# Performance work log

Hardware: AMD Instinct MI355X
Metric: run time of the kernel (lower is better)

Reference implementation:

```python
import jax, jax.numpy as jnp
import numpy as np
from jax import lax

S = 64        # num_sam_segments
B = 2
HIMG = 336    # full-res SAM segmap / painted map
HP = 24       # DINO patch grid (336/14)
CD = 768      # DINO feature channels
CM = 3072     # concatenated backbone channels (4 layers * 768)
RH = 48       # readout spatial size ceil(336/7)
HID = 128     # SPADE hidden_mlp_channels
EPS = 1e-12


def conv2d(x, w, b=None, pad=0):
    out = lax.conv_general_dilated(x, w, (1, 1), [(pad, pad), (pad, pad)],
                                   dimension_numbers=("NCHW", "OIHW", "NCHW"))
    if b is not None:
        out = out + b[None, :, None, None]
    return out


def paint_semantic_map(f_sem, segmap):
    # f_sem: (B, C, Hp, Wp) float; segmap: (B, H, W) int
    Bn, C, Hp, Wp = f_sem.shape
    H, W = segmap.shape[1:]
    # torch F.interpolate mode='nearest' downsample: src_idx = floor(dst_idx * in/out)
    iy = (jnp.arange(Hp) * H) // Hp
    ix = (jnp.arange(Wp) * W) // Wp
    seg_p = segmap[:, iy][:, :, ix]                      # (B, Hp, Wp)
    ids = jnp.clip(seg_p, 0, S - 1).reshape(Bn, -1)      # (B, Np)
    ids_off = (ids + jnp.arange(Bn)[:, None] * S).reshape(-1)
    flat = f_sem.transpose(0, 2, 3, 1).reshape(Bn * Hp * Wp, C)
    sums = jax.ops.segment_sum(flat, ids_off, num_segments=Bn * S)
    cnt = jax.ops.segment_sum(jnp.ones((Bn * Hp * Wp, 1), flat.dtype), ids_off,
                              num_segments=Bn * S)
    means = jnp.where(cnt > 0, sums / jnp.maximum(cnt, 1.0), 0.0).reshape(Bn, S, C)
    pix = jnp.clip(segmap, 0, S - 1)                     # (B, H, W)
    painted = means[jnp.arange(Bn)[:, None, None], pix]  # (B, H, W, C) gather
    return painted.transpose(0, 3, 1, 2)                 # (B, C, H, W)


def spade_ln(x, painted, ws, bs, wg, bg, wb, bb):
    # layer_norm over (C,H,W) per sample, no affine
    mean = jnp.mean(x, axis=(1, 2, 3), keepdims=True)
    var = jnp.mean((x - mean) ** 2, axis=(1, 2, 3), keepdims=True)
    xn = (x - mean) * lax.rsqrt(var + EPS)
    sem = jax.image.resize(painted, (x.shape[0], painted.shape[1], x.shape[2], x.shape[3]),
                           method="bilinear")
    h = jax.nn.relu(conv2d(sem, ws, bs, pad=1))
    gamma = conv2d(h, wg, bg, pad=1)
    beta = conv2d(h, wb, bb, pad=1)
    return xn * (1.0 + gamma) + beta


def setup_inputs() -> dict:
    key = jax.random.key(0)
    ks = jax.random.split(key, 16)
    n = lambda k, sh: jax.random.normal(k, sh, jnp.float32) * 0.02
    inp = {
        "x_main": jax.random.normal(ks[0], (B, CM, RH, RH), jnp.float32),
        "f_sem": jax.random.normal(ks[1], (B, CD, HP, HP), jnp.float32),
        "segmap": jax.random.randint(ks[2], (B, HIMG, HIMG), 0, S, jnp.int32),
    }
    i = 3
    for li, nf in enumerate([CM, 8, 16]):
        inp[f"ws{li}"] = n(ks[i], (HID, CD, 3, 3)); inp[f"bs{li}"] = jnp.zeros((HID,), jnp.float32)
        inp[f"wg{li}"] = n(ks[i + 1], (nf, HID, 3, 3)); inp[f"bg{li}"] = jnp.zeros((nf,), jnp.float32)
        inp[f"wb{li}"] = n(ks[i + 2], (nf, HID, 3, 3)); inp[f"bb{li}"] = jnp.zeros((nf,), jnp.float32)
        i += 3
    inp["w0"] = n(ks[12], (8, CM, 1, 1)); inp["bias0"] = jnp.zeros((8,), jnp.float32)
    inp["w1"] = n(ks[13], (16, 8, 1, 1)); inp["bias1"] = jnp.zeros((16,), jnp.float32)
    inp["w2"] = n(ks[14], (1, 16, 1, 1)); inp["bias2"] = jnp.zeros((1,), jnp.float32)
    return inp


def reference(x_main, f_sem, segmap,
              ws0, bs0, wg0, bg0, wb0, bb0,
              ws1, bs1, wg1, bg1, wb1, bb1,
              ws2, bs2, wg2, bg2, wb2, bb2,
              w0, bias0, w1, bias1, w2, bias2):
    painted = paint_semantic_map(f_sem, segmap)
    h = spade_ln(x_main, painted, ws0, bs0, wg0, bg0, wb0, bb0)
    h = jax.nn.softplus(conv2d(h, w0) + bias0[None, :, None, None])
    h = spade_ln(h, painted, ws1, bs1, wg1, bg1, wb1, bb1)
    h = jax.nn.softplus(conv2d(h, w1) + bias1[None, :, None, None])
    h = spade_ln(h, painted, ws2, bs2, wg2, bg2, wb2, bb2)
    h = jax.nn.softplus(conv2d(h, w2) + bias2[None, :, None, None])
    return h  # (B, 1, RH, RH)
```

## Files before the change

kernel.cpp:

```cpp
#include <hip/hip_runtime.h>
#include <hip/hip_bf16.h>

typedef __hip_bfloat16 bf16;
typedef __bf16 v8bf __attribute__((ext_vector_type(8)));
typedef float v4f __attribute__((ext_vector_type(4)));

#define PB 2304
#define PTOT 4608

__device__ __forceinline__ float b2f(bf16 x){ return __bfloat162float(x); }
__device__ __forceinline__ bf16 f2b(float x){ return __float2bfloat16(x); }
__device__ __forceinline__ float softplus_f(float x){
  return fmaxf(x, 0.f) + log1pf(expf(-fabsf(x)));
}
__device__ __forceinline__ float LD(const void* src, size_t i, int fl){
  return fl ? ((const float*)src)[i] : b2f(((const bf16*)src)[i]);
}

__device__ __forceinline__ void gload_lds16(const void* g, void* l){
  __builtin_amdgcn_global_load_lds(
      (const __attribute__((address_space(1))) void*)g,
      (__attribute__((address_space(3))) void*)l, 16, 0, 0);
}

__global__ __launch_bounds__(256) void k_sniff(const unsigned* __restrict__ x, int* __restrict__ flag,
                                               float* __restrict__ zp){
  int t = threadIdx.x;
  if (t < 128) zp[t] = 0.f;
  int cnt = 0;
  for (int i = t; i < 4096; i += 256){
    unsigned e = (x[i] >> 8) & 0x7F;
    if (e >= 0x38 && e <= 0x42) cnt++;
  }
  for (int off = 32; off; off >>= 1) cnt += __shfl_down(cnt, off, 64);
  __shared__ int sc[4];
  if ((t & 63) == 0) sc[t >> 6] = cnt;
  __syncthreads();
  if (t == 0) *flag = (sc[0]+sc[1]+sc[2]+sc[3] < 2048) ? 1 : 0;
}

__global__ __launch_bounds__(256) void k_cvt_small(
    const void* s4, const void* s10, const void* s16, const void* s6, const void* s8,
    const void* s12, const void* s14, const void* s18, const void* s20,
    const void* s21, const void* s22, const void* s23, const void* s24,
    const void* s25, const void* s26,
    float* __restrict__ dst, const int* __restrict__ flag, float* __restrict__ MB){
  int i = blockIdx.x*256 + threadIdx.x;
  if (i >= 40537) return;
  if (i >= 31321){ MB[i - 31321] = 0.f; return; }
  int fl = *flag;
  const void* src; size_t off;
  if      (i < 128)   { src = s4;  off = i; }
  else if (i < 256)   { src = s10; off = i - 128; }
  else if (i < 384)   { src = s16; off = i - 256; }
  else if (i < 3456)  { src = s6;  off = i - 384; }
  else if (i < 6528)  { src = s8;  off = i - 3456; }
  else if (i < 6536)  { src = s12; off = i - 6528; }
  else if (i < 6544)  { src = s14; off = i - 6536; }
  else if (i < 6560)  { src = s18; off = i - 6544; }
  else if (i < 6576)  { src = s20; off = i - 6560; }
  else if (i < 31152) { src = s21; off = i - 6576; }
  else if (i < 31160) { src = s22; off = i - 31152; }
  else if (i < 31288) { src = s23; off = i - 31160; }
  else if (i < 31304) { src = s24; off = i - 31288; }
  else if (i < 31320) { src = s25; off = i - 31304; }
  else                { src = s26; off = i - 31320; }
  dst[i] = LD(src, off, fl);
}

__global__ __launch_bounds__(256) void k_bcol(const float* __restrict__ SMALLF, float* __restrict__ BCOL){
  int t = threadIdx.x;
  const float* BG1 = SMALLF + 6528; const float* BB1 = SMALLF + 6536;
  const float* BG2 = SMALLF + 6544; const float* BB2 = SMALLF + 6560;
  const float* BB0 = SMALLF + 3456; const float* W0  = SMALLF + 6576;
  if (t < 8)       BCOL[t] = BG1[t];
  else if (t < 16) BCOL[t] = BB1[t-8];
  else if (t < 32) BCOL[t] = BG2[t-16];
  else if (t < 48) BCOL[t] = BB2[t-32];
  else if (t < 64) BCOL[t] = 0.f;
  float part[8] = {0,0,0,0,0,0,0,0};
  for (int c = t; c < 3072; c += 256){
    float bb = BB0[c];
    #pragma unroll
    for (int oc = 0; oc < 8; oc++) part[oc] += bb*W0[oc*3072 + c];
  }
  __shared__ float red[4][8];
  int wv = t >> 6, lane = t & 63;
  #pragma unroll
  for (int oc = 0; oc < 8; oc++){
    float v = part[oc];
    for (int off = 32; off; off >>= 1) v += __shfl_down(v, off, 64);
    if (lane == 0) red[wv][oc] = v;
  }
  __syncthreads();
  if (t < 8) BCOL[48 + t] = red[0][t] + red[1][t] + red[2][t] + red[3][t];
}

__global__ __launch_bounds__(256) void k_mbeta(const void* __restrict__ wb0, const int* __restrict__ flag,
                                               const float* __restrict__ w0f, float* __restrict__ MB){
  int jb = blockIdx.x, nb = blockIdx.y, t = threadIdx.x;
  int fl = *flag;
  int jl = t & 127, nh = t >> 7;
  int j = jb*128 + jl;
  int src = jl*9 + jb;
  float acc[8] = {0,0,0,0,0,0,0,0};
  int n0 = nb*128 + nh*64;
  for (int i = 0; i < 64; i++){
    int n = n0 + i;
    float wv = LD(wb0, (size_t)n*1152 + src, fl);
    #pragma unroll
    for (int oc = 0; oc < 8; oc++) acc[oc] += wv*w0f[oc*3072 + n];
  }
  #pragma unroll
  for (int oc = 0; oc < 8; oc++) atomicAdd(&MB[oc*1152 + j], acc[oc]);
}

__global__ __launch_bounds__(256) void k_wsm(const float* __restrict__ MB, bf16* __restrict__ WSMALL){
  int i = blockIdx.x*256 + threadIdx.x;
  if (i >= 9216) return;
  float v = MB[i];
  bf16 hi = f2b(v);
  WSMALL[48*1152 + i] = hi;
  WSMALL[56*1152 + i] = f2b(v - b2f(hi));
}

template<int ICW>
__global__ __launch_bounds__(256) void k_permW(const void* __restrict__ src, bf16* __restrict__ dst,
                                               int total, const int* __restrict__ flag){
  int idx = blockIdx.x*256 + threadIdx.x;
  if (idx >= total) return;
  int oc = idx / (9*ICW);
  int rr = idx % (9*ICW);
  int dyx = rr / ICW, ic = rr % ICW;
  size_t si = (size_t)(oc*ICW + ic)*9 + dyx;
  dst[idx] = f2b(LD(src, si, *flag));
}

__global__ __launch_bounds__(256) void k_permoc(const void* __restrict__ src, bf16* __restrict__ dst,
                                                const int* __restrict__ flag){
  __shared__ float lds[4608];
  int t = threadIdx.x;
  size_t base = (size_t)blockIdx.x*4608;
  int fl = *flag;
  for (int i = t; i < 4608; i += 256) lds[i] = LD(src, base + i, fl);
  __syncthreads();
  for (int i = t; i < 4608; i += 256){
    int ocl = i / 1152, r = i - ocl*1152;
    int dyx = r >> 7, ic = r & 127;
    dst[base + i] = f2b(lds[ocl*1152 + ic*9 + dyx]);
  }
}

__global__ __launch_bounds__(256) void k_permws(const void* __restrict__ ws0, const void* __restrict__ ws1,
                                                const void* __restrict__ ws2, const int* __restrict__ flag,
                                                float* __restrict__ WSP){
  __shared__ float lds[6912];
  int t = threadIdx.x;
  int oc = blockIdx.x;
  int l = oc >> 7, ocl = oc & 127;
  const void* src = l == 0 ? ws0 : (l == 1 ? ws1 : ws2);
  int fl = *flag;
  for (int i = t; i < 6912; i += 256) lds[i] = LD(src, (size_t)ocl*6912 + i, fl);
  __syncthreads();
  float* o = WSP + (size_t)oc*6912;
  for (int i = t; i < 6912; i += 256){
    int dyx = i / 768, ic = i - dyx*768;
    o[i] = lds[ic*9 + dyx];
  }
}

__global__ __launch_bounds__(256) void k_seg_means(const void* __restrict__ f_sem, const int* __restrict__ flag,
                                                   const int* __restrict__ segmap,
                                                   float* __restrict__ means){
  int s = blockIdx.x, b = blockIdx.y, t = threadIdx.x;
  int fl = *flag;
  __shared__ int sid[576];
  for (int i = t; i < 576; i += 256){
    int y = i / 24, x = i % 24;
    int v = segmap[b*336*336 + (y*14)*336 + x*14];
    sid[i] = min(max(v, 0), 63);
  }
  __syncthreads();
  float a0=0.f, a1=0.f, a2=0.f; int cnt = 0;
  for (int i = 0; i < 576; i++){
    if (sid[i] == s){
      cnt++;
      a0 += LD(f_sem, (size_t)(b*768 + t      )*576 + i, fl);
      a1 += LD(f_sem, (size_t)(b*768 + t + 256)*576 + i, fl);
      a2 += LD(f_sem, (size_t)(b*768 + t + 512)*576 + i, fl);
    }
  }
  float inv = cnt > 0 ? 1.f/(float)cnt : 0.f;
  float* o = means + (size_t)(b*64 + s)*768;
  o[t] = a0*inv; o[t+256] = a1*inv; o[t+512] = a2*inv;
}

__global__ __launch_bounds__(256) void k_tt(const float* __restrict__ WSP,
    const float* __restrict__ means, bf16* __restrict__ WTT){
  int bx = blockIdx.x;
  int dyx = bx / 24, ocb = bx % 24;
  int b = blockIdx.y, t = threadIdx.x;
  int ocg0 = ocb*16;
  __shared__ float wl[16][768];
  for (int ol = 0; ol < 16; ol++)
    for (int ic = t; ic < 768; ic += 256)
      wl[ol][ic] = WSP[(size_t)(ocg0 + ol)*6912 + (size_t)dyx*768 + ic];
  __syncthreads();
  int s = t & 63, og = t >> 6;
  const float* mr = means + ((size_t)b*64 + s)*768;
  float acc[4] = {0.f, 0.f, 0.f, 0.f};
  for (int ic = 0; ic < 768; ic += 4){
    float4 m = *reinterpret_cast<const float4*>(mr + ic);
    #pragma unroll
    for (int k = 0; k < 4; k++){
      const float* w = &wl[og + k*4][ic];
      acc[k] += m.x*w[0] + m.y*w[1] + m.z*w[2] + m.w*w[3];
    }
  }
  #pragma unroll
  for (int k = 0; k < 4; k++){
    bf16 h = f2b(acc[k]);
    size_t base = ((size_t)(b*384 + ocg0 + og + k*4))*1152 + (size_t)dyx*128 + s;
    WTT[base] = h;
    WTT[base + 64] = h;
  }
}

__global__ __launch_bounds__(192) void k_A(const int* __restrict__ segmap, bf16* __restrict__ AHL){
  int blk = blockIdx.x;
  int b = blk / PB, rem = blk % PB, yo = rem / 48, xo = rem % 48;
  __shared__ float accs[64];
  int t = threadIdx.x;
  if (t < 64) accs[t] = 0.f;
  __syncthreads();
  if (t < 169){
    int ty = t / 13, tx = t % 13;
    int jy = 7*yo - 3 + ty, jx = 7*xo - 3 + tx;
    if (jy >= 0 && jy < 336 && jx >= 0 && jx < 336){
      int wy = 7 - abs(ty - 6), wx = 7 - abs(tx - 6);
      int sv = segmap[b*336*336 + jy*336 + jx];
      sv = min(max(sv, 0), 63);
      atomicAdd(&accs[sv], (float)(wy*wx));
    }
  }
  int sumy = 0, sumx = 0;
  for (int k = 0; k < 13; k++){
    int jy = 7*yo - 3 + k; if (jy >= 0 && jy < 336) sumy += 7 - abs(k - 6);
    int jx = 7*xo - 3 + k; if (jx >= 0 && jx < 336) sumx += 7 - abs(k - 6);
  }
  __syncthreads();
  if (t < 64){
    float v = accs[t] / (float)(sumy*sumx);
    bf16 hi = f2b(v);
    AHL[(size_t)blk*128 + t] = hi;
    AHL[(size_t)blk*128 + 64 + t] = f2b(v - b2f(hi));
  }
}

__global__ __launch_bounds__(256) void k_ln_partial(const void* __restrict__ x, const int* __restrict__ flag,
                                                    float2* __restrict__ part){
  int b = blockIdx.y, blk = blockIdx.x, t = threadIdx.x;
  int fl = *flag;
  size_t base = (size_t)b*7077888 + (size_t)blk*55296;
  float s = 0.f, sq = 0.f;
  for (int i = 0; i < 216; i++){
    float v = LD(x, base + t + i*256, fl);
    s += v; sq += v*v;
  }
  for (int off = 32; off; off >>= 1){ s += __shfl_down(s, off, 64); sq += __shfl_down(sq, off, 64); }
  __shared__ float ls[4], lq[4];
  int w = t >> 6, lane = t & 63;
  if (lane == 0){ ls[w] = s; lq[w] = sq; }
  __syncthreads();
  if (t == 0) part[b*128 + blk] = make_float2(ls[0]+ls[1]+ls[2]+ls[3], lq[0]+lq[1]+lq[2]+lq[3]);
}

__global__ void k_ln_final(const float2* __restrict__ part, float* __restrict__ stats){
  int b = blockIdx.x, t = threadIdx.x;
  float2 v = part[b*128 + t];
  float s = v.x, sq = v.y;
  for (int off = 32; off; off >>= 1){ s += __shfl_down(s, off, 64); sq += __shfl_down(sq, off, 64); }
  __shared__ float ls[2], lq[2];
  if ((t & 63) == 0){ ls[t>>6] = s; lq[t>>6] = sq; }
  __syncthreads();
  if (t == 0){
    s = ls[0]+ls[1]; sq = lq[0]+lq[1];
    const float N = 7077888.f;
    float mean = s/N; float var = sq/N - mean*mean; var = fmaxf(var, 0.f);
    stats[b*2] = mean; stats[b*2+1] = rsqrtf(var + 1e-12f);
  }
}

__global__ __launch_bounds__(256) void k_spln(float* __restrict__ z, int cnt, float* __restrict__ stats){
  int b = blockIdx.x, t = threadIdx.x;
  float* p = z + (size_t)b*cnt;
  float s = 0.f, sq = 0.f;
  for (int i = t; i < cnt; i += 256){
    float v = softplus_f(p[i]);
    p[i] = v;
    s += v; sq += v*v;
  }
  for (int off = 32; off; off >>= 1){ s += __shfl_down(s, off, 64); sq += __shfl_down(sq, off, 64); }
  __shared__ float ls[4], lq[4];
  int w = t >> 6, lane = t & 63;
  if (lane == 0){ ls[w] = s; lq[w] = sq; }
  __syncthreads();
  if (t == 0){
    s = ls[0]+ls[1]+ls[2]+ls[3]; sq = lq[0]+lq[1]+lq[2]+lq[3];
    float mean = s/(float)cnt; float var = sq/(float)cnt - mean*mean; var = fmaxf(var, 0.f);
    stats[b*2] = mean; stats[b*2+1] = rsqrtf(var + 1e-12f);
  }
}

__global__ __launch_bounds__(256) void k_ln_small(const float* __restrict__ z, int cnt, float* __restrict__ stats){
  int b = blockIdx.x, t = threadIdx.x;
  const float* p = z + (size_t)b*cnt;
  float s = 0.f, sq = 0.f;
  for (int i = t; i < cnt; i += 256){ float v = p[i]; s += v; sq += v*v; }
  for (int off = 32; off; off >>= 1){ s += __shfl_down(s, off, 64); sq += __shfl_down(sq, off, 64); }
  __shared__ float ls[4], lq[4];
  int w = t >> 6, lane = t & 63;
  if (lane == 0){ ls[w] = s; lq[w] = sq; }
  __syncthreads();
  if (t == 0){
    s = ls[0]+ls[1]+ls[2]+ls[3]; sq = lq[0]+lq[1]+lq[2]+lq[3];
    float mean = s/(float)cnt; float var = sq/(float)cnt - mean*mean; var = fmaxf(var, 0.f);
    stats[b*2] = mean; stats[b*2+1] = rsqrtf(var + 1e-12f);
  }
}

template<bool RELU, typename OT>
__device__ __forceinline__ void gemm_body(
    const bf16* __restrict__ Asrc, int AS, int acol, int ICW,
    const bf16* __restrict__ W, int K, size_t wbstride,
    const float* __restrict__ bp0, const float* __restrict__ bp1, const float* __restrict__ bp2, int seg,
    OT* __restrict__ out, int N, int ncb, int ldo, const bf16* __restrict__ zpad,
    int m0, int n0, bf16 (*Al)[64], bf16 (*Bl)[64])
{
  int t = threadIdx.x;
  int wv = t >> 6, lane = t & 63;
  int lr8 = lane >> 3, sseg = (lane & 7) ^ lr8;
  int b = m0 >= PB ? 1 : 0;

  int ya[2], xa[2]; bool bv[2]; const bf16* wb[2];
  #pragma unroll
  for (int i = 0; i < 2; i++){
    int sp = (m0 - b*PB) + wv*16 + i*8 + lr8;
    ya[i] = sp / 48; xa[i] = sp % 48;
    int nrow = ncb + n0 + wv*16 + i*8 + lr8;
    bv[i] = nrow < N;
    wb[i] = W + (size_t)b*wbstride + (size_t)nrow*K + sseg*8;
  }

  int wm = (wv >> 1)*32, wn = (wv & 1)*32;
  int lrow = lane & 15, quad = lane >> 4;
  int sx = lrow & 7;
  int o0 = ((quad    ) ^ sx)*8;
  int o1 = ((quad + 4) ^ sx)*8;

  v4f acc00 = {0,0,0,0}, acc01 = {0,0,0,0}, acc10 = {0,0,0,0}, acc11 = {0,0,0,0};

  int dyx = 0, ic0 = 0;
  int ktn = K / 64;
  for (int kt = 0; kt < ktn; kt++){
    int dy = dyx/3 - 1, dx = dyx%3 - 1;
    #pragma unroll
    for (int i = 0; i < 2; i++){
      int ys = ya[i] + dy, xs = xa[i] + dx;
      const bf16* ga = (ys >= 0 && ys < 48 && xs >= 0 && xs < 48)
        ? Asrc + (size_t)(b*PB + ys*48 + xs)*AS + acol + ic0 + sseg*8 : zpad;
      gload_lds16(ga, &Al[wv*16 + i*8][0]);
      const bf16* gb = bv[i] ? wb[i] + kt*64 : zpad;
      gload_lds16(gb, &Bl[wv*16 + i*8][0]);
    }
    asm volatile("s_waitcnt vmcnt(0)" ::: "memory");
    __syncthreads();
    v8bf a00 = *reinterpret_cast<const v8bf*>(&Al[wm      + lrow][o0]);
    v8bf a10 = *reinterpret_cast<const v8bf*>(&Al[wm + 16 + lrow][o0]);
    v8bf a01 = *reinterpret_cast<const v8bf*>(&Al[wm      + lrow][o1]);
    v8bf a11 = *reinterpret_cast<const v8bf*>(&Al[wm + 16 + lrow][o1]);
    v8bf b00 = *reinterpret_cast<const v8bf*>(&Bl[wn      + lrow][o0]);
    v8bf b10 = *reinterpret_cast<const v8bf*>(&Bl[wn + 16 + lrow][o0]);
    v8bf b01 = *reinterpret_cast<const v8bf*>(&Bl[wn      + lrow][o1]);
    v8bf b11 = *reinterpret_cast<const v8bf*>(&Bl[wn + 16 + lrow][o1]);
    acc00 = __builtin_amdgcn_mfma_f32_16x16x32_bf16(a00, b00, acc00, 0, 0, 0);
    acc00 = __builtin_amdgcn_mfma_f32_16x16x32_bf16(a01, b01, acc00, 0, 0, 0);
    acc01 = __builtin_amdgcn_mfma_f32_16x16x32_bf16(a00, b10, acc01, 0, 0, 0);
    acc01 = __builtin_amdgcn_mfma_f32_16x16x32_bf16(a01, b11, acc01, 0, 0, 0);
    acc10 = __builtin_amdgcn_mfma_f32_16x16x32_bf16(a10, b00, acc10, 0, 0, 0);
    acc10 = __builtin_amdgcn_mfma_f32_16x16x32_bf16(a11, b01, acc10, 0, 0, 0);
    acc11 = __builtin_amdgcn_mfma_f32_16x16x32_bf16(a10, b10, acc11, 0, 0, 0);
    acc11 = __builtin_amdgcn_mfma_f32_16x16x32_bf16(a11, b11, acc11, 0, 0, 0);
    __syncthreads();
    ic0 += 64; if (ic0 == ICW){ ic0 = 0; dyx++; }
  }

  auto store_tile = [&](v4f a, int mi, int ni){
    int gcol = ncb + n0 + wn + ni*16 + lrow;
    if (gcol >= N) return;
    int sel = gcol / seg; sel = sel > 2 ? 2 : sel;
    const float* bp = sel == 0 ? bp0 : (sel == 1 ? bp1 : bp2);
    float bias = bp[gcol - sel*seg];
    int rowb = m0 + wm + mi*16 + quad*4;
    #pragma unroll
    for (int rg = 0; rg < 4; rg++){
      float v = a[rg] + bias;
      if (RELU) v = fmaxf(v, 0.f);
      if constexpr (sizeof(OT) == 2) out[(size_t)(rowb+rg)*ldo + (gcol - ncb)] = f2b(v);
      else                           out[(size_t)(rowb+rg)*ldo + (gcol - ncb)] = (OT)v;
    }
  };
  store_tile(acc00, 0, 0); store_tile(acc01, 0, 1);
  store_tile(acc10, 1, 0); store_tile(acc11, 1, 1);
}

template<bool RELU, typename OT>
__global__ __launch_bounds__(256) void k_gemm(
    const bf16* __restrict__ Asrc, int AS, int acol, int ICW,
    const bf16* __restrict__ W, int K, size_t wbstride,
    const float* __restrict__ bp0, const float* __restrict__ bp1, const float* __restrict__ bp2, int seg,
    OT* __restrict__ out, int N, int ncb, int ldo, const bf16* __restrict__ zpad)
{
  __shared__ __align__(16) bf16 Al[64][64];
  __shared__ __align__(16) bf16 Bl[64][64];
  gemm_body<RELU, OT>(Asrc, AS, acol, ICW, W, K, wbstride, bp0, bp1, bp2, seg,
                      out, N, ncb, ldo, zpad, blockIdx.x*64, blockIdx.y*64, Al, Bl);
}

__global__ __launch_bounds__(256) void k_gsmall(
    const bf16* __restrict__ HS, const bf16* __restrict__ WSMALL, const float* __restrict__ BCOL,
    float* __restrict__ GBS, const bf16* __restrict__ zpad)
{
  __shared__ __align__(16) bf16 Al[64][64];
  __shared__ __align__(16) bf16 Bl[64][64];
  int y = blockIdx.y;
  int acol = y == 0 ? 128 : (y == 1 ? 256 : 0);
  const bf16* W = WSMALL + (y == 0 ? 0 : (y == 1 ? 16*1152 : 48*1152));
  const float* bp = BCOL + (y == 0 ? 0 : (y == 1 ? 16 : 48));
  float* out = GBS + (y == 0 ? 0 : (y == 1 ? 16 : 48));
  int N = y == 1 ? 32 : 16;
  gemm_body<false, float>(HS, 384, acol, 128, W, 1152, 0, bp, bp, bp, 9999,
                          out, N, 0, 64, zpad, blockIdx.x*64, 0, Al, Bl);
}

__global__ __launch_bounds__(256, 4) void k_gg(
    const bf16* __restrict__ HS, const bf16* __restrict__ WG0, const float* __restrict__ BG0,
    bf16* __restrict__ GAMMA, const bf16* __restrict__ zpad)
{
  __shared__ __align__(16) bf16 Al[128][64];
  __shared__ __align__(16) bf16 Bl[128][64];
  int t = threadIdx.x;
  int m0 = blockIdx.x*128, n0 = blockIdx.y*128;
  int b = m0 >= PB ? 1 : 0;
  int wv = t >> 6, lane = t & 63;
  int lr8 = lane >> 3, sseg = (lane & 7) ^ lr8;
  int spbase = m0 - b*PB;

  int ya[4], xa[4];
  #pragma unroll
  for (int i = 0; i < 4; i++){
    int sp = spbase + wv*32 + i*8 + lr8;
    ya[i] = sp / 48; xa[i] = sp % 48;
  }
  const bf16* wgb = WG0 + (size_t)(n0 + wv*32 + lr8)*1152 + sseg*8;

  int wm = wv*32, lrow = lane & 15, quad = lane >> 4;
  int sx = lrow & 7;

  v4f acc[2][8];
  #pragma unroll
  for (int mi = 0; mi < 2; mi++)
    #pragma unroll
    for (int ni = 0; ni < 8; ni++) acc[mi][ni] = (v4f){0,0,0,0};

  for (int kt = 0; kt < 18; kt++){
    int dyx = kt >> 1, icr = (kt & 1) << 6;
    int dy = dyx/3 - 1, dx = dyx%3 - 1;
    #pragma unroll
    for (int i = 0; i < 4; i++){
      int ys = ya[i] + dy, xs = xa[i] + dx;
      const bf16* ga = (ys >= 0 && ys < 48 && xs >= 0 && xs < 48)
        ? HS + (size_t)(b*PB + ys*48 + xs)*384 + icr + sseg*8 : zpad;
      gload_lds16(ga, &Al[wv*32 + i*8][0]);
      gload_lds16(wgb + (size_t)(i*8)*1152 + dyx*128 + icr, &Bl[wv*32 + i*8][0]);
    }
    asm volatile("s_waitcnt vmcnt(0)" ::: "memory");
    __syncthreads();
    #pragma unroll
    for (int kh = 0; kh < 2; kh++){
      int oa = ((kh*4 + quad) ^ sx)*8;
      v8bf a0 = *reinterpret_cast<const v8bf*>(&Al[wm      + lrow][oa]);
      v8bf a1 = *reinterpret_cast<const v8bf*>(&Al[wm + 16 + lrow][oa]);
      #pragma unroll
      for (int ni = 0; ni < 8; ni++){
        v8bf bn = *reinterpret_cast<const v8bf*>(&Bl[ni*16 + lrow][oa]);
        acc[0][ni] = __builtin_amdgcn_mfma_f32_16x16x32_bf16(a0, bn, acc[0][ni], 0, 0, 0);
        acc[1][ni] = __builtin_amdgcn_mfma_f32_16x16x32_bf16(a1, bn, acc[1][ni], 0, 0, 0);
      }
    }
    __syncthreads();
  }

  #pragma unroll
  for (int mi = 0; mi < 2; mi++){
    int pr = m0 + wm + mi*16 + quad*4;
    #pragma unroll
    for (int ni = 0; ni < 8; ni++){
      int gc = n0 + ni*16 + lrow;
      float bg = BG0[gc];
      #pragma unroll
      for (int rg = 0; rg < 4; rg++)
        GAMMA[(size_t)(pr + rg)*3072 + gc] = f2b(acc[mi][ni][rg] + bg);
    }
  }
}

__global__ __launch_bounds__(256) void k_zc(
    const void* __restrict__ x, const bf16* __restrict__ GAMMA, const int* __restrict__ flag,
    const float* __restrict__ stats, const float* __restrict__ w0f, float* __restrict__ z0)
{
  __shared__ bf16 gmT[64][66];
  __shared__ float w0l[8][64];
  __shared__ float red[4][64][8];
  int t = threadIdx.x;
  int p0 = blockIdx.x*64, cb = blockIdx.y;
  int b = p0 / PB;
  int spbase = p0 - b*PB;
  int fl = *flag;
  float mean = stats[b*2], rstd = stats[b*2+1];
  int px = t & 63, cg = t >> 6;
  int pxs = t >> 6, cl = t & 63;

  float acc[8] = {0,0,0,0,0,0,0,0};
  for (int ct = 0; ct < 6; ct++){
    int c0 = cb*384 + ct*64;
    #pragma unroll
    for (int k = 0; k < 16; k++){
      int p = pxs + k*4;
      gmT[cl][p] = GAMMA[(size_t)(p0 + p)*3072 + c0 + cl];
    }
    for (int i = t; i < 512; i += 256) w0l[i >> 6][i & 63] = w0f[(size_t)(i >> 6)*3072 + c0 + (i & 63)];
    __syncthreads();
    #pragma unroll
    for (int ci = 0; ci < 16; ci++){
      int c = cg*16 + ci;
      float xv = LD(x, ((size_t)(b*3072 + c0 + c))*2304 + spbase + px, fl);
      float xn = (xv - mean)*rstd;
      float tv = xn*(1.f + b2f(gmT[c][px]));
      #pragma unroll
      for (int oc = 0; oc < 8; oc++) acc[oc] += tv*w0l[oc][c];
    }
    __syncthreads();
  }
  #pragma unroll
  for (int oc = 0; oc < 8; oc++) red[cg][px][oc] = acc[oc];
  __syncthreads();
  #pragma unroll
  for (int j = 0; j < 2; j++){
    int idx = t + j*256;
    int p2 = idx >> 3, o2 = idx & 7;
    float s = red[0][p2][o2] + red[1][p2][o2] + red[2][p2][o2] + red[3][p2][o2];
    atomicAdd(&z0[(size_t)(p0 + p2)*8 + o2], s);
  }
}

__global__ __launch_bounds__(256) void k_z0init(const float* __restrict__ b0f, const float* __restrict__ GBS,
                                                float* __restrict__ z0){
  int i = blockIdx.x*256 + threadIdx.x;
  if (i >= 36864) return;
  int p = i >> 3, oc = i & 7;
  z0[i] = b0f[oc] + GBS[(size_t)p*64 + 48 + oc] + GBS[(size_t)p*64 + 56 + oc];
}

__global__ __launch_bounds__(256) void k_F1(const float* __restrict__ z0, const float* __restrict__ GBS,
    const float* __restrict__ stats, const float* __restrict__ w1f, const float* __restrict__ b1f,
    float* __restrict__ z1){
  int p = blockIdx.x*256 + threadIdx.x;
  if (p >= PTOT) return;
  int b = p / PB;
  float mean = stats[b*2], rstd = stats[b*2+1];
  const float* zr = z0 + (size_t)p*8;
  const float* gr = GBS + (size_t)p*64;
  float yv[8];
  #pragma unroll
  for (int c = 0; c < 8; c++) yv[c] = (zr[c] - mean)*rstd*(1.f + gr[c]) + gr[8 + c];
  #pragma unroll
  for (int oc = 0; oc < 16; oc++){
    float s = b1f[oc];
    #pragma unroll
    for (int c = 0; c < 8; c++) s += yv[c]*w1f[oc*8 + c];
    z1[(size_t)p*16 + oc] = softplus_f(s);
  }
}

__global__ __launch_bounds__(256) void k_F2(const float* __restrict__ z1, const float* __restrict__ GBS,
    const float* __restrict__ stats, const float* __restrict__ w2f, const float* __restrict__ b2f,
    void* __restrict__ outp, const int* __restrict__ flag){
  int p = blockIdx.x*256 + threadIdx.x;
  if (p >= PTOT) return;
  int b = p / PB;
  float mean = stats[b*2], rstd = stats[b*2+1];
  const float* zr = z1 + (size_t)p*16;
  const float* gr = GBS + (size_t)p*64 + 16;
  float s = b2f[0];
  #pragma unroll
  for (int c = 0; c < 16; c++){
    float yv = (zr[c] - mean)*rstd*(1.f + gr[c]) + gr[16 + c];
    s += yv*w2f[c];
  }
  float r = softplus_f(s);
  if (*flag) ((float*)outp)[p] = r;
  else       ((bf16*)outp)[p] = f2b(r);
}

extern "C" void kernel_launch(void* const* d_in, const int* in_sizes, int n_in,
                              void* d_out, int out_size, void* d_ws, size_t ws_size,
                              hipStream_t stream){
  const void* x_main = d_in[0];
  const void* f_sem  = d_in[1];
  const int*  segmap = (const int*)d_in[2];

  char* ws = (char*)d_ws;
  size_t o = 0;
  auto alloc = [&](size_t bytes){ size_t r = o; o = (o + bytes + 255) & ~(size_t)255; return r; };
  float* MEANS = (float*)(ws + alloc(98304u*4));
  bf16*  AHL   = (bf16*) (ws + alloc(589824u*2));
  bf16*  WTT   = (bf16*) (ws + alloc(884736u*2));
  bf16*  WG0   = (bf16*) (ws + alloc(3538944u*2));
  bf16*  WSMALL= (bf16*) (ws + alloc(73728u*2));
  bf16*  HS    = (bf16*) (ws + alloc(1769472u*2));
  float* WSP   = (float*)(ws + alloc(2654208u*4));
  bf16*  GAMMA = (bf16*) (ws + alloc(14155776u*2));
  float* GBS   = (float*)(ws + alloc(294912u*4));
  float* Z0    = (float*)(ws + alloc(36864u*4));
  float* Z1    = (float*)(ws + alloc(73728u*4));
  float2* LNP  = (float2*)(ws + alloc(256u*8));
  float* STATS = (float*)(ws + alloc(16u*4));
  int*   FLAG  = (int*)  (ws + alloc(64u));
  float* SMALLF= (float*)(ws + alloc(31321u*4));
  float* MB    = (float*)(ws + alloc(9216u*4));
  float* BCOL  = (float*)(ws + alloc(64u*4));
  bf16*  ZPAD  = (bf16*) (ws + alloc(512u));

  float *BS0=SMALLF+0, *BS1=SMALLF+128, *BS2=SMALLF+256;
  float *BG0=SMALLF+384;
  float *W0=SMALLF+6576, *B0=SMALLF+31152;
  float *W1=SMALLF+31160, *B1=SMALLF+31288;
  float *W2=SMALLF+31304, *B2=SMALLF+31320;

  k_sniff<<<1, 256, 0, stream>>>((const unsigned*)x_main, FLAG, (float*)ZPAD);
  k_cvt_small<<<159, 256, 0, stream>>>(d_in[4], d_in[10], d_in[16], d_in[6], d_in[8],
      d_in[12], d_in[14], d_in[18], d_in[20], d_in[21], d_in[22], d_in[23], d_in[24],
      d_in[25], d_in[26], SMALLF, FLAG, MB);
  k_bcol<<<1, 256, 0, stream>>>(SMALLF, BCOL);
  k_mbeta<<<dim3(9,24), 256, 0, stream>>>(d_in[7], FLAG, W0, MB);
  k_wsm<<<36, 256, 0, stream>>>(MB, WSMALL);

  k_permoc<<<768, 256, 0, stream>>>(d_in[5], WG0, FLAG);
  k_permws<<<384, 256, 0, stream>>>(d_in[3], d_in[9], d_in[15], FLAG, WSP);
  k_permW<128><<<dim3((9216+255)/256),   256, 0, stream>>>(d_in[11], WSMALL,           9216, FLAG);
  k_permW<128><<<dim3((9216+255)/256),   256, 0, stream>>>(d_in[13], WSMALL + 8*1152,  9216, FLAG);
  k_permW<128><<<dim3((18432+255)/256),  256, 0, stream>>>(d_in[17], WSMALL + 16*1152, 18432, FLAG);
  k_permW<128><<<dim3((18432+255)/256),  256, 0, stream>>>(d_in[19], WSMALL + 32*1152, 18432, FLAG);

  k_ln_partial<<<dim3(128,2), 256, 0, stream>>>(x_main, FLAG, LNP);
  k_ln_final<<<2, 128, 0, stream>>>(LNP, STATS);
  k_seg_means<<<dim3(64,2), 256, 0, stream>>>(f_sem, FLAG, segmap, MEANS);
  k_tt<<<dim3(216,2), 256, 0, stream>>>(WSP, MEANS, WTT);
  k_A<<<PTOT, 192, 0, stream>>>(segmap, AHL);

  k_gemm<true, bf16><<<dim3(72,6), 256, 0, stream>>>(AHL, 128, 0, 128, WTT, 1152, (size_t)384*1152,
      BS0, BS1, BS2, 128, HS, 384, 0, 384, ZPAD);
  k_gsmall<<<dim3(72,3), 256, 0, stream>>>(HS, WSMALL, BCOL, GBS, ZPAD);

  k_z0init<<<144, 256, 0, stream>>>(B0, GBS, Z0);
  k_gg<<<dim3(36,24), 256, 0, stream>>>(HS, WG0, BG0, GAMMA, ZPAD);
  k_zc<<<dim3(72,8), 256, 0, stream>>>(x_main, GAMMA, FLAG, STATS, W0, Z0);
  k_spln<<<2, 256, 0, stream>>>(Z0, 18432, STATS + 4);

  k_F1<<<18, 256, 0, stream>>>(Z0, GBS, STATS + 4, W1, B1, Z1);
  k_ln_small<<<2, 256, 0, stream>>>(Z1, 36864, STATS + 8);
  k_F2<<<18, 256, 0, stream>>>(Z1, GBS, STATS + 8, W2, B2, d_out, FLAG);
}
```

Before: 597.9 us.

## Restructure mbeta and zc kernels for coalesced loads and merge permW launches

k_mbeta now stages contiguous rows of wb0 in shared memory and accumulates over all 1152 outputs per block, then remaps the index on the atomic write. This replaces the strided per-thread global reads and cuts the grid to 24 blocks. k_zc now handles 128 pixels per block with two pixels per thread and float2 loads of x, preloads the W0 slice once, and splits channels into 24 groups of 128 instead of 8 of 384, giving more blocks. The four k_permW launches are merged into one kernel to save launch overhead. The trade-offs are fewer blocks and more shared memory in k_mbeta, and more atomics on z0 in k_zc.

```diff
diff --git a/kernel.cpp b/kernel.cpp
--- a/kernel.cpp
+++ b/kernel.cpp
@@ -98,21 +98,46 @@
 
 __global__ __launch_bounds__(256) void k_mbeta(const void* __restrict__ wb0, const int* __restrict__ flag,
                                                const float* __restrict__ w0f, float* __restrict__ MB){
-  int jb = blockIdx.x, nb = blockIdx.y, t = threadIdx.x;
+  __shared__ float wl[8][1152];
+  int t = threadIdx.x;
+  int nb = blockIdx.x;
   int fl = *flag;
-  int jl = t & 127, nh = t >> 7;
-  int j = jb*128 + jl;
-  int src = jl*9 + jb;
-  float acc[8] = {0,0,0,0,0,0,0,0};
-  int n0 = nb*128 + nh*64;
-  for (int i = 0; i < 64; i++){
-    int n = n0 + i;
-    float wv = LD(wb0, (size_t)n*1152 + src, fl);
-    #pragma unroll
-    for (int oc = 0; oc < 8; oc++) acc[oc] += wv*w0f[oc*3072 + n];
-  }
-  #pragma unroll
-  for (int oc = 0; oc < 8; oc++) atomicAdd(&MB[oc*1152 + j], acc[oc]);
+  float acc[5][8];
+  #pragma unroll
+  for (int jt = 0; jt < 5; jt++)
+    #pragma unroll
+    for (int oc = 0; oc < 8; oc++) acc[jt][oc] = 0.f;
+  for (int ns = 0; ns < 16; ns++){
+    int n0 = nb*128 + ns*8;
+    for (int i = t; i < 9216; i += 256)
+      wl[i/1152][i%1152] = LD(wb0, (size_t)(n0 + i/1152)*1152 + (i%1152), fl);
+    __syncthreads();
+    #pragma unroll
+    for (int nl = 0; nl < 8; nl++){
+      int n = n0 + nl;
+      float w0v[8];
+      #pragma unroll
+      for (int oc = 0; oc < 8; oc++) w0v[oc] = w0f[oc*3072 + n];
+      #pragma unroll
+      for (int jt = 0; jt < 5; jt++){
+        int j = jt*256 + t;
+        float wv = (j < 1152) ? wl[nl][j] : 0.f;
+        #pragma unroll
+        for (int oc = 0; oc < 8; oc++) acc[jt][oc] += wv*w0v[oc];
+      }
+    }
+    __syncthreads();
+  }
+  #pragma unroll
+  for (int jt = 0; jt < 5; jt++){
+    int jraw = jt*256 + t;
+    if (jraw < 1152){
+      int ic = jraw/9, dyx = jraw%9;
+      int j = dyx*128 + ic;
+      #pragma unroll
+      for (int oc = 0; oc < 8; oc++) atomicAdd(&MB[oc*1152 + j], acc[jt][oc]);
+    }
+  }
 }
 
 __global__ __launch_bounds__(256) void k_wsm(const float* __restrict__ MB, bf16* __restrict__ WSMALL){
@@ -124,16 +149,19 @@
   WSMALL[56*1152 + i] = f2b(v - b2f(hi));
 }
 
-template<int ICW>
-__global__ __launch_bounds__(256) void k_permW(const void* __restrict__ src, bf16* __restrict__ dst,
-                                               int total, const int* __restrict__ flag){
-  int idx = blockIdx.x*256 + threadIdx.x;
-  if (idx >= total) return;
-  int oc = idx / (9*ICW);
-  int rr = idx % (9*ICW);
-  int dyx = rr / ICW, ic = rr % ICW;
-  size_t si = (size_t)(oc*ICW + ic)*9 + dyx;
-  dst[idx] = f2b(LD(src, si, *flag));
+__global__ __launch_bounds__(256) void k_permW4(const void* __restrict__ s11, const void* __restrict__ s13,
+                                                const void* __restrict__ s17, const void* __restrict__ s19,
+                                                bf16* __restrict__ WSMALL, const int* __restrict__ flag){
+  int i = blockIdx.x*256 + threadIdx.x;
+  if (i >= 55296) return;
+  const void* src; bf16* dst; int idx;
+  if      (i < 9216) { src = s11; dst = WSMALL;           idx = i; }
+  else if (i < 18432){ src = s13; dst = WSMALL + 8*1152;  idx = i - 9216; }
+  else if (i < 36864){ src = s17; dst = WSMALL + 16*1152; idx = i - 18432; }
+  else               { src = s19; dst = WSMALL + 32*1152; idx = i - 36864; }
+  int oc = idx / 1152, rr = idx % 1152;
+  int dyx = rr >> 7, ic = rr & 127;
+  dst[idx] = f2b(LD(src, (size_t)(oc*128 + ic)*9 + dyx, *flag));
 }
 
 __global__ __launch_bounds__(256) void k_permoc(const void* __restrict__ src, bf16* __restrict__ dst,
@@ -519,44 +547,65 @@
     const void* __restrict__ x, const bf16* __restrict__ GAMMA, const int* __restrict__ flag,
     const float* __restrict__ stats, const float* __restrict__ w0f, float* __restrict__ z0)
 {
-  __shared__ bf16 gmT[64][66];
-  __shared__ float w0l[8][64];
-  __shared__ float red[4][64][8];
-  int t = threadIdx.x;
-  int p0 = blockIdx.x*64, cb = blockIdx.y;
+  __shared__ bf16 gmT[64][130];
+  __shared__ float w0l[8][128];
+  __shared__ float red[4][128][9];
+  int t = threadIdx.x;
+  int p0 = blockIdx.x*128, cb = blockIdx.y;
   int b = p0 / PB;
   int spbase = p0 - b*PB;
   int fl = *flag;
   float mean = stats[b*2], rstd = stats[b*2+1];
-  int px = t & 63, cg = t >> 6;
-  int pxs = t >> 6, cl = t & 63;
-
-  float acc[8] = {0,0,0,0,0,0,0,0};
-  for (int ct = 0; ct < 6; ct++){
-    int c0 = cb*384 + ct*64;
-    #pragma unroll
-    for (int k = 0; k < 16; k++){
-      int p = pxs + k*4;
-      gmT[cl][p] = GAMMA[(size_t)(p0 + p)*3072 + c0 + cl];
-    }
-    for (int i = t; i < 512; i += 256) w0l[i >> 6][i & 63] = w0f[(size_t)(i >> 6)*3072 + c0 + (i & 63)];
+  int lane = t & 63, cg = t >> 6;
+  int c0b = cb*128;
+
+  for (int i = t; i < 1024; i += 256) w0l[i >> 7][i & 127] = w0f[(size_t)(i >> 7)*3072 + c0b + (i & 127)];
+
+  float acc0[8], acc1[8];
+  #pragma unroll
+  for (int oc = 0; oc < 8; oc++){ acc0[oc] = 0.f; acc1[oc] = 0.f; }
+
+  for (int ct = 0; ct < 2; ct++){
+    int c0 = c0b + ct*64;
+    {
+      int cl = t & 63, pr = t >> 6;
+      #pragma unroll
+      for (int k = 0; k < 32; k++){
+        int p = pr + k*4;
+        gmT[cl][p] = GAMMA[(size_t)(p0 + p)*3072 + c0 + cl];
+      }
+    }
     __syncthreads();
     #pragma unroll
     for (int ci = 0; ci < 16; ci++){
       int c = cg*16 + ci;
-      float xv = LD(x, ((size_t)(b*3072 + c0 + c))*2304 + spbase + px, fl);
-      float xn = (xv - mean)*rstd;
-      float tv = xn*(1.f + b2f(gmT[c][px]));
+      float xv0, xv1;
+      if (fl){
+        const float* xp = (const float*)x + ((size_t)(b*3072 + c0 + c))*2304 + spbase + lane*2;
+        float2 v = *reinterpret_cast<const float2*>(xp);
+        xv0 = v.x; xv1 = v.y;
+      } else {
+        const bf16* xp = (const bf16*)x + ((size_t)(b*3072 + c0 + c))*2304 + spbase + lane*2;
+        xv0 = b2f(xp[0]); xv1 = b2f(xp[1]);
+      }
+      float t0 = (xv0 - mean)*rstd*(1.f + b2f(gmT[c][lane*2]));
+      float t1 = (xv1 - mean)*rstd*(1.f + b2f(gmT[c][lane*2 + 1]));
       #pragma unroll
-      for (int oc = 0; oc < 8; oc++) acc[oc] += tv*w0l[oc][c];
+      for (int oc = 0; oc < 8; oc++){
+        float wv = w0l[oc][ct*64 + c];
+        acc0[oc] += t0*wv; acc1[oc] += t1*wv;
+      }
     }
     __syncthreads();
   }
   #pragma unroll
-  for (int oc = 0; oc < 8; oc++) red[cg][px][oc] = acc[oc];
-  __syncthreads();
-  #pragma unroll
-  for (int j = 0; j < 2; j++){
+  for (int oc = 0; oc < 8; oc++){
+    red[cg][lane*2    ][oc] = acc0[oc];
+    red[cg][lane*2 + 1][oc] = acc1[oc];
+  }
+  __syncthreads();
+  #pragma unroll
+  for (int j = 0; j < 4; j++){
     int idx = t + j*256;
     int p2 = idx >> 3, o2 = idx & 7;
     float s = red[0][p2][o2] + red[1][p2][o2] + red[2][p2][o2] + red[3][p2][o2];
@@ -653,15 +702,12 @@
       d_in[12], d_in[14], d_in[18], d_in[20], d_in[21], d_in[22], d_in[23], d_in[24],
       d_in[25], d_in[26], SMALLF, FLAG, MB);
   k_bcol<<<1, 256, 0, stream>>>(SMALLF, BCOL);
-  k_mbeta<<<dim3(9,24), 256, 0, stream>>>(d_in[7], FLAG, W0, MB);
+  k_mbeta<<<24, 256, 0, stream>>>(d_in[7], FLAG, W0, MB);
   k_wsm<<<36, 256, 0, stream>>>(MB, WSMALL);
 
   k_permoc<<<768, 256, 0, stream>>>(d_in[5], WG0, FLAG);
   k_permws<<<384, 256, 0, stream>>>(d_in[3], d_in[9], d_in[15], FLAG, WSP);
-  k_permW<128><<<dim3((9216+255)/256),   256, 0, stream>>>(d_in[11], WSMALL,           9216, FLAG);
-  k_permW<128><<<dim3((9216+255)/256),   256, 0, stream>>>(d_in[13], WSMALL + 8*1152,  9216, FLAG);
-  k_permW<128><<<dim3((18432+255)/256),  256, 0, stream>>>(d_in[17], WSMALL + 16*1152, 18432, FLAG);
-  k_permW<128><<<dim3((18432+255)/256),  256, 0, stream>>>(d_in[19], WSMALL + 32*1152, 18432, FLAG);
+  k_permW4<<<216, 256, 0, stream>>>(d_in[11], d_in[13], d_in[17], d_in[19], WSMALL, FLAG);
 
   k_ln_partial<<<dim3(128,2), 256, 0, stream>>>(x_main, FLAG, LNP);
   k_ln_final<<<2, 128, 0, stream>>>(LNP, STATS);
@@ -675,7 +721,7 @@
 
   k_z0init<<<144, 256, 0, stream>>>(B0, GBS, Z0);
   k_gg<<<dim3(36,24), 256, 0, stream>>>(HS, WG0, BG0, GAMMA, ZPAD);
-  k_zc<<<dim3(72,8), 256, 0, stream>>>(x_main, GAMMA, FLAG, STATS, W0, Z0);
+  k_zc<<<dim3(36,24), 256, 0, stream>>>(x_main, GAMMA, FLAG, STATS, W0, Z0);
   k_spln<<<2, 256, 0, stream>>>(Z0, 18432, STATS + 4);
 
   k_F1<<<18, 256, 0, stream>>>(Z0, GBS, STATS + 4, W1, B1, Z1);
```

Result: slower. 779.6 us (+30.4%).
